# Performance work log

Measured on AMD Instinct MI355X. Metric: run time of the kernel, lower is better.

The kernel has to match this reference:

```python
import jax, jax.numpy as jnp
import numpy as np

B, L, A, HD, H = 4096, 512, 64, 1024, 32
EPS = 1e-5


def _ln(x, g, b):
    m = jnp.mean(x, axis=-1, keepdims=True)
    v = jnp.mean((x - m) ** 2, axis=-1, keepdims=True)
    return (x - m) * jax.lax.rsqrt(v + EPS) * g + b


def setup_inputs() -> dict:
    key = jax.random.key(0)
    ks = jax.random.split(key, 12)
    s = 0.02
    return {
        "z_0": jax.random.normal(ks[0], (B, L), jnp.float32),
        "actions": jax.random.normal(ks[1], (B, H, A), jnp.float32),
        "W1": jax.random.normal(ks[2], (L + A, HD), jnp.float32) * s,
        "b1": jnp.zeros((HD,), jnp.float32),
        "g1": jnp.ones((HD,), jnp.float32),
        "be1": jnp.zeros((HD,), jnp.float32),
        "W2": jax.random.normal(ks[3], (HD, HD), jnp.float32) * s,
        "b2": jnp.zeros((HD,), jnp.float32),
        "g2": jnp.ones((HD,), jnp.float32),
        "be2": jnp.zeros((HD,), jnp.float32),
        "W3": jax.random.normal(ks[4], (HD, L), jnp.float32) * s,
        "b3": jnp.zeros((L,), jnp.float32),
        "uW1": jax.random.normal(ks[5], (L, HD // 2), jnp.float32) * s,
        "ub1": jnp.zeros((HD // 2,), jnp.float32),
        "uW2": jax.random.normal(ks[6], (HD // 2, 1), jnp.float32) * s,
        "ub2": jnp.zeros((1,), jnp.float32),
        "gate": jnp.asarray(0.5, jnp.float32),
    }


def reference(z_0, actions, W1, b1, g1, be1, W2, b2, g2, be2, W3, b3,
              uW1, ub1, uW2, ub2, gate):
    gate_s = jax.nn.sigmoid(gate)

    def step_fn(z, a):
        za = jnp.concatenate([z, a], axis=-1)              # [B, L+A]
        h = jax.nn.gelu(_ln(za @ W1 + b1, g1, be1), approximate=False)
        h = jax.nn.gelu(_ln(h @ W2 + b2, g2, be2), approximate=False)
        dz = h @ W3 + b3                                   # [B, L]
        z_next = z + gate_s * dz
        u = jax.nn.gelu(z_next @ uW1 + ub1, approximate=False)
        sigma = jax.nn.softplus(u @ uW2 + ub2)             # [B, 1]
        return z_next, (z_next, sigma)

    a_seq = jnp.swapaxes(actions, 0, 1)                    # [H, B, A]
    _, (traj, sigs) = jax.lax.scan(step_fn, z_0, a_seq)
    return jnp.swapaxes(traj, 0, 1), jnp.swapaxes(sigs, 0, 1)
```

## Files before the change

kernel.cpp:

```cpp
#include <hip/hip_runtime.h>
#include <hip/hip_bf16.h>
#include <math.h>

#define B_SZ 4096
#define L_SZ 512
#define A_SZ 64
#define HD_SZ 1024
#define H_SZ 32

typedef __attribute__((ext_vector_type(8))) short bf16x8;
typedef __attribute__((ext_vector_type(4))) short s16x4;
typedef __attribute__((ext_vector_type(4))) float f32x4;

union frag_u { bf16x8 v; s16x4 h[2]; };

#define GLDS16(gsrc, ldst) __builtin_amdgcn_global_load_lds(              \
    (const __attribute__((address_space(1))) void*)(gsrc),                \
    (__attribute__((address_space(3))) void*)(ldst), 16, 0, 0)

__device__ __forceinline__ float gelu_exact(float x) {
  return 0.5f * x * (1.0f + erff(x * 0.70710678118654752f));
}

template <int BM, int BN, int MODE>
__global__ __launch_bounds__(256, 2) void gemm_kernel(
    const __hip_bfloat16* __restrict__ A0, int a0s,
    const __hip_bfloat16* __restrict__ A1, int a1s, int ksplit,
    const __hip_bfloat16* __restrict__ Bt,
    const float* __restrict__ bias,
    int N, int K,
    float* __restrict__ outf,
    float* __restrict__ z_cur,
    __hip_bfloat16* __restrict__ znb,
    float* __restrict__ traj,
    const float* __restrict__ gate,
    int t,
    const float* __restrict__ uW2,
    float* __restrict__ sig_acc) {
  constexpr int BK = 64;
  constexpr int FM = BM / 32, FN = BN / 32;
  constexpr int HALF = (BM + BN) * BK;
  __shared__ __align__(16) __hip_bfloat16 lds[2 * HALF];

  const int tid = threadIdx.x;
  const int m0 = blockIdx.x * BM, n0 = blockIdx.y * BN;
  const int wave = tid >> 6, lane = tid & 63;
  const int l15 = lane & 15, lg = lane >> 4;
  const int wm = wave >> 1, wn = wave & 1;
  const int NK = K / BK;

  f32x4 acc[FM][FN];
#pragma unroll
  for (int mi = 0; mi < FM; ++mi)
#pragma unroll
    for (int ni = 0; ni < FN; ++ni) acc[mi][ni] = (f32x4){0.f, 0.f, 0.f, 0.f};

  auto stage = [&](int buf, int kt) {
    __hip_bfloat16* dA = lds + buf * HALF;
    __hip_bfloat16* dB = dA + BM * BK;
    const int k0 = kt * BK;
    const __hip_bfloat16* Aptr;
    int As, kloc;
    if (k0 < ksplit) { Aptr = A0; As = a0s; kloc = k0; }
    else             { Aptr = A1; As = a1s; kloc = k0 - ksplit; }
#pragma unroll
    for (int i = 0; i < BM / 32; ++i) {
      int off = tid * 16 + i * 4096;
      int r = off >> 7, c = off & 127;
      int csw = c ^ ((r & 7) << 4);
      GLDS16(Aptr + (size_t)(m0 + r) * As + kloc + (csw >> 1), dA + (off >> 1));
    }
#pragma unroll
    for (int i = 0; i < BN / 32; ++i) {
      int off = tid * 16 + i * 4096;
      int r = off >> 7, c = off & 127;
      int csw = c ^ ((r & 7) << 4);
      GLDS16(Bt + (size_t)(n0 + r) * K + k0 + (csw >> 1), dB + (off >> 1));
    }
  };

  stage(0, 0);
  asm volatile("s_waitcnt vmcnt(0)" ::: "memory");
  __syncthreads();

  int buf = 0;
  for (int kt = 0; kt < NK; ++kt) {
    if (kt + 1 < NK) stage(buf ^ 1, kt + 1);

    const __hip_bfloat16* ldsA = lds + buf * HALF;
    const __hip_bfloat16* ldsB = ldsA + BM * BK;

    frag_u a_[FM][2], b_[FN][2];
#pragma unroll
    for (int mi = 0; mi < FM; ++mi) {
      int row = wm * (FM * 16) + mi * 16 + l15;
      int xr = (row & 7) << 4;
      const char* base = (const char*)(ldsA + row * BK);
#pragma unroll
      for (int s = 0; s < 2; ++s) {
        a_[mi][s].h[0] = *(const s16x4*)(base + ((s * 64 + lg * 8) ^ xr));
        a_[mi][s].h[1] = *(const s16x4*)(base + ((s * 64 + 32 + lg * 8) ^ xr));
      }
    }
#pragma unroll
    for (int ni = 0; ni < FN; ++ni) {
      int row = wn * (FN * 16) + ni * 16 + l15;
      int xr = (row & 7) << 4;
      const char* base = (const char*)(ldsB + row * BK);
#pragma unroll
      for (int s = 0; s < 2; ++s) {
        b_[ni][s].h[0] = *(const s16x4*)(base + ((s * 64 + lg * 8) ^ xr));
        b_[ni][s].h[1] = *(const s16x4*)(base + ((s * 64 + 32 + lg * 8) ^ xr));
      }
    }
#pragma unroll
    for (int s = 0; s < 2; ++s)
#pragma unroll
      for (int mi = 0; mi < FM; ++mi)
#pragma unroll
        for (int ni = 0; ni < FN; ++ni)
          acc[mi][ni] = __builtin_amdgcn_mfma_f32_16x16x32_bf16(
              a_[mi][s].v, b_[ni][s].v, acc[mi][ni], 0, 0, 0);

    asm volatile("s_waitcnt vmcnt(0)" ::: "memory");
    __syncthreads();
    buf ^= 1;
  }

  if constexpr (MODE == 3) {
#pragma unroll
    for (int mi = 0; mi < FM; ++mi) {
      float p[4] = {0.f, 0.f, 0.f, 0.f};
#pragma unroll
      for (int ni = 0; ni < FN; ++ni) {
        int gcol = n0 + wn * (FN * 16) + ni * 16 + l15;
        float bv = bias[gcol];
        float w2 = uW2[gcol];
#pragma unroll
        for (int r = 0; r < 4; ++r)
          p[r] += gelu_exact(acc[mi][ni][r] + bv) * w2;
      }
#pragma unroll
      for (int o = 1; o < 16; o <<= 1) {
#pragma unroll
        for (int r = 0; r < 4; ++r) p[r] += __shfl_xor(p[r], o);
      }
      if (l15 == 0) {
        int rowb = m0 + wm * (FM * 16) + mi * 16 + lg * 4;
#pragma unroll
        for (int r = 0; r < 4; ++r)
          atomicAdd(&sig_acc[(size_t)(rowb + r) * H_SZ + t], p[r]);
      }
    }
  } else {
    float gs = 0.f;
    if constexpr (MODE == 1) gs = 1.f / (1.f + expf(-gate[0]));
#pragma unroll
    for (int mi = 0; mi < FM; ++mi) {
#pragma unroll
      for (int ni = 0; ni < FN; ++ni) {
        int gcol = n0 + wn * (FN * 16) + ni * 16 + l15;
        float bv = bias[gcol];
#pragma unroll
        for (int r = 0; r < 4; ++r) {
          int grow = m0 + wm * (FM * 16) + mi * 16 + lg * 4 + r;
          float v = acc[mi][ni][r] + bv;
          if constexpr (MODE == 0) {
            outf[(size_t)grow * N + gcol] = v;
          } else {
            size_t zi = (size_t)grow * L_SZ + gcol;
            float zn = z_cur[zi] + gs * v;
            z_cur[zi] = zn;
            znb[zi] = __float2bfloat16(zn);
            traj[(size_t)grow * (H_SZ * L_SZ) + (size_t)t * L_SZ + gcol] = zn;
          }
        }
      }
    }
  }
}

__global__ __launch_bounds__(256) void ln_gelu_kernel(
    const float* __restrict__ x, const float* __restrict__ gam,
    const float* __restrict__ bet, __hip_bfloat16* __restrict__ out) {
  constexpr int N = HD_SZ;
  const int row = blockIdx.x;
  const int tid = threadIdx.x, lane = tid & 63, wave = tid >> 6;
  const float* xr = x + (size_t)row * N;
  f32x4 v = *(const f32x4*)(xr + tid * 4);
  float s = v[0] + v[1] + v[2] + v[3];
  float s2 = v[0] * v[0] + v[1] * v[1] + v[2] * v[2] + v[3] * v[3];
#pragma unroll
  for (int o = 32; o; o >>= 1) {
    s += __shfl_xor(s, o);
    s2 += __shfl_xor(s2, o);
  }
  __shared__ float as_[4], as2_[4];
  if (lane == 0) { as_[wave] = s; as2_[wave] = s2; }
  __syncthreads();
  s = as_[0] + as_[1] + as_[2] + as_[3];
  s2 = as2_[0] + as2_[1] + as2_[2] + as2_[3];
  float mean = s * (1.f / N);
  float var = s2 * (1.f / N) - mean * mean;
  float rstd = rsqrtf(var + 1e-5f);
  f32x4 g = *(const f32x4*)(gam + tid * 4);
  f32x4 b = *(const f32x4*)(bet + tid * 4);
  union { __hip_bfloat16 h[4]; s16x4 sv; } o;
#pragma unroll
  for (int j = 0; j < 4; ++j) {
    float y = (v[j] - mean) * rstd * g[j] + b[j];
    o.h[j] = __float2bfloat16(gelu_exact(y));
  }
  *(s16x4*)(out + (size_t)row * N + tid * 4) = o.sv;
}

__global__ void transpose_cvt(const float* __restrict__ in,
                              __hip_bfloat16* __restrict__ out, int K, int N) {
  __shared__ float tile[32][33];
  const int n0 = blockIdx.x * 32, k0 = blockIdx.y * 32;
  const int tx = threadIdx.x, ty = threadIdx.y;
#pragma unroll
  for (int i = 0; i < 32; i += 8)
    tile[ty + i][tx] = in[(size_t)(k0 + ty + i) * N + (n0 + tx)];
  __syncthreads();
#pragma unroll
  for (int i = 0; i < 32; i += 8)
    out[(size_t)(n0 + ty + i) * K + (k0 + tx)] = __float2bfloat16(tile[tx][ty + i]);
}

__global__ void cvt_bf16_kernel(const float* __restrict__ in,
                                __hip_bfloat16* __restrict__ out, int n4) {
  int i = blockIdx.x * 256 + threadIdx.x;
  if (i >= n4) return;
  f32x4 v = ((const f32x4*)in)[i];
  union { __hip_bfloat16 h[4]; s16x4 sv; } o;
#pragma unroll
  for (int j = 0; j < 4; ++j) o.h[j] = __float2bfloat16(v[j]);
  ((s16x4*)out)[i] = o.sv;
}

__global__ void init_z_kernel(const float* __restrict__ z0,
                              float* __restrict__ z_cur,
                              __hip_bfloat16* __restrict__ znb, int n4) {
  int i = blockIdx.x * 256 + threadIdx.x;
  if (i >= n4) return;
  f32x4 v = ((const f32x4*)z0)[i];
  ((f32x4*)z_cur)[i] = v;
  union { __hip_bfloat16 h[4]; s16x4 sv; } o;
#pragma unroll
  for (int j = 0; j < 4; ++j) o.h[j] = __float2bfloat16(v[j]);
  ((s16x4*)znb)[i] = o.sv;
}

__global__ void zero_kernel(float* __restrict__ p, int n) {
  int i = blockIdx.x * 256 + threadIdx.x;
  if (i < n) p[i] = 0.f;
}

__global__ void softplus_kernel(const float* __restrict__ acc,
                                const float* __restrict__ ub2,
                                float* __restrict__ out, int n) {
  int i = blockIdx.x * 256 + threadIdx.x;
  if (i >= n) return;
  float v = acc[i] + ub2[0];
  out[i] = v > 20.f ? v : log1pf(expf(v));
}

extern "C" void kernel_launch(void* const* d_in, const int* in_sizes, int n_in,
                              void* d_out, int out_size, void* d_ws,
                              size_t ws_size, hipStream_t stream) {
  const float* z0      = (const float*)d_in[0];
  const float* actions = (const float*)d_in[1];
  const float* W1  = (const float*)d_in[2];
  const float* b1  = (const float*)d_in[3];
  const float* g1  = (const float*)d_in[4];
  const float* be1 = (const float*)d_in[5];
  const float* W2  = (const float*)d_in[6];
  const float* b2  = (const float*)d_in[7];
  const float* g2  = (const float*)d_in[8];
  const float* be2 = (const float*)d_in[9];
  const float* W3  = (const float*)d_in[10];
  const float* b3  = (const float*)d_in[11];
  const float* uW1 = (const float*)d_in[12];
  const float* ub1 = (const float*)d_in[13];
  const float* uW2 = (const float*)d_in[14];
  const float* ub2 = (const float*)d_in[15];
  const float* gate = (const float*)d_in[16];

  char* w = (char*)d_ws;
  __hip_bfloat16* W1t = (__hip_bfloat16*)w;  w += (size_t)(L_SZ + A_SZ) * HD_SZ * 2;
  __hip_bfloat16* W2t = (__hip_bfloat16*)w;  w += (size_t)HD_SZ * HD_SZ * 2;
  __hip_bfloat16* W3t = (__hip_bfloat16*)w;  w += (size_t)HD_SZ * L_SZ * 2;
  __hip_bfloat16* uW1t = (__hip_bfloat16*)w; w += (size_t)L_SZ * (HD_SZ / 2) * 2;
  __hip_bfloat16* actb = (__hip_bfloat16*)w; w += (size_t)B_SZ * H_SZ * A_SZ * 2;
  float* z_cur = (float*)w;                  w += (size_t)B_SZ * L_SZ * 4;
  __hip_bfloat16* znb = (__hip_bfloat16*)w;  w += (size_t)B_SZ * L_SZ * 2;
  float* tws = (float*)w;                    w += (size_t)B_SZ * HD_SZ * 4;
  __hip_bfloat16* hb = (__hip_bfloat16*)w;   w += (size_t)B_SZ * HD_SZ * 2;
  float* sig_acc = (float*)w;                w += (size_t)B_SZ * H_SZ * 4;

  float* trajOut = (float*)d_out;
  float* sigsOut = (float*)d_out + (size_t)B_SZ * H_SZ * L_SZ;

  dim3 tb(32, 8);
  transpose_cvt<<<dim3(HD_SZ / 32, (L_SZ + A_SZ) / 32), tb, 0, stream>>>(W1, W1t, L_SZ + A_SZ, HD_SZ);
  transpose_cvt<<<dim3(HD_SZ / 32, HD_SZ / 32), tb, 0, stream>>>(W2, W2t, HD_SZ, HD_SZ);
  transpose_cvt<<<dim3(L_SZ / 32, HD_SZ / 32), tb, 0, stream>>>(W3, W3t, HD_SZ, L_SZ);
  transpose_cvt<<<dim3((HD_SZ / 2) / 32, L_SZ / 32), tb, 0, stream>>>(uW1, uW1t, L_SZ, HD_SZ / 2);

  cvt_bf16_kernel<<<(B_SZ * H_SZ * A_SZ / 4 + 255) / 256, 256, 0, stream>>>(
      actions, actb, B_SZ * H_SZ * A_SZ / 4);
  init_z_kernel<<<(B_SZ * L_SZ / 4 + 255) / 256, 256, 0, stream>>>(
      z0, z_cur, znb, B_SZ * L_SZ / 4);
  zero_kernel<<<(B_SZ * H_SZ + 255) / 256, 256, 0, stream>>>(sig_acc, B_SZ * H_SZ);

  const int KSPLIT_NONE = 1 << 30;
  for (int t = 0; t < H_SZ; ++t) {
    gemm_kernel<64, 128, 0><<<dim3(B_SZ / 64, HD_SZ / 128), 256, 0, stream>>>(
        znb, L_SZ, actb + (size_t)t * A_SZ, H_SZ * A_SZ, L_SZ, W1t, b1,
        HD_SZ, L_SZ + A_SZ, tws, nullptr, nullptr, nullptr, nullptr, 0,
        nullptr, nullptr);
    ln_gelu_kernel<<<B_SZ, 256, 0, stream>>>(tws, g1, be1, hb);
    gemm_kernel<64, 128, 0><<<dim3(B_SZ / 64, HD_SZ / 128), 256, 0, stream>>>(
        hb, HD_SZ, nullptr, 0, KSPLIT_NONE, W2t, b2,
        HD_SZ, HD_SZ, tws, nullptr, nullptr, nullptr, nullptr, 0,
        nullptr, nullptr);
    ln_gelu_kernel<<<B_SZ, 256, 0, stream>>>(tws, g2, be2, hb);
    gemm_kernel<32, 128, 1><<<dim3(B_SZ / 32, L_SZ / 128), 256, 0, stream>>>(
        hb, HD_SZ, nullptr, 0, KSPLIT_NONE, W3t, b3,
        L_SZ, HD_SZ, nullptr, z_cur, znb, trajOut, gate, t,
        nullptr, nullptr);
    gemm_kernel<32, 128, 3><<<dim3(B_SZ / 32, (HD_SZ / 2) / 128), 256, 0, stream>>>(
        znb, L_SZ, nullptr, 0, KSPLIT_NONE, uW1t, ub1,
        HD_SZ / 2, L_SZ, nullptr, nullptr, nullptr, nullptr, nullptr, t,
        uW2, sig_acc);
  }
  softplus_kernel<<<(B_SZ * H_SZ + 255) / 256, 256, 0, stream>>>(
      sig_acc, ub2, sigsOut, B_SZ * H_SZ);
}
```

Baseline: 2.518 ms.

## Switch GEMM to triple-buffered BK=32 pipeline with counted waits and larger tiles

Restructures the GEMM main loop from a double-buffered BK=64 scheme to a three-stage LDS ring with BK=32. It issues loads two tiles ahead and uses counted vmcnt waits instead of draining all outstanding loads each iteration. LDS fragment reads become single 16-byte loads with a simpler swizzle, and all four GEMM launches double their M tile (128x128 and 64x128). The aim is to keep more global loads in flight and raise MFMA work per block, at the cost of more barriers per K step and fewer blocks in each grid.

```diff
diff --git a/kernel.cpp b/kernel.cpp
--- a/kernel.cpp
+++ b/kernel.cpp
@@ -12,11 +12,13 @@
 typedef __attribute__((ext_vector_type(4))) short s16x4;
 typedef __attribute__((ext_vector_type(4))) float f32x4;
 
-union frag_u { bf16x8 v; s16x4 h[2]; };
-
 #define GLDS16(gsrc, ldst) __builtin_amdgcn_global_load_lds(              \
     (const __attribute__((address_space(1))) void*)(gsrc),                \
     (__attribute__((address_space(3))) void*)(ldst), 16, 0, 0)
+
+template <int N> __device__ __forceinline__ void vmwait() {
+  asm volatile("s_waitcnt vmcnt(%0)" :: "n"(N) : "memory");
+}
 
 __device__ __forceinline__ float gelu_exact(float x) {
   return 0.5f * x * (1.0f + erff(x * 0.70710678118654752f));
@@ -37,10 +39,12 @@
     int t,
     const float* __restrict__ uW2,
     float* __restrict__ sig_acc) {
-  constexpr int BK = 64;
+  constexpr int BK = 32;
   constexpr int FM = BM / 32, FN = BN / 32;
-  constexpr int HALF = (BM + BN) * BK;
-  __shared__ __align__(16) __hip_bfloat16 lds[2 * HALF];
+  constexpr int ABYTES = BM * 64;
+  constexpr int BUFB = (BM + BN) * 64;
+  constexpr int LOADS = (BM + BN) / 64;
+  __shared__ __align__(16) char lds[3 * BUFB];
 
   const int tid = threadIdx.x;
   const int m0 = blockIdx.x * BM, n0 = blockIdx.y * BN;
@@ -56,75 +60,65 @@
     for (int ni = 0; ni < FN; ++ni) acc[mi][ni] = (f32x4){0.f, 0.f, 0.f, 0.f};
 
   auto stage = [&](int buf, int kt) {
-    __hip_bfloat16* dA = lds + buf * HALF;
-    __hip_bfloat16* dB = dA + BM * BK;
+    char* dst = lds + buf * BUFB;
     const int k0 = kt * BK;
     const __hip_bfloat16* Aptr;
     int As, kloc;
     if (k0 < ksplit) { Aptr = A0; As = a0s; kloc = k0; }
     else             { Aptr = A1; As = a1s; kloc = k0 - ksplit; }
 #pragma unroll
-    for (int i = 0; i < BM / 32; ++i) {
+    for (int i = 0; i < BM / 64; ++i) {
       int off = tid * 16 + i * 4096;
-      int r = off >> 7, c = off & 127;
-      int csw = c ^ ((r & 7) << 4);
-      GLDS16(Aptr + (size_t)(m0 + r) * As + kloc + (csw >> 1), dA + (off >> 1));
-    }
-#pragma unroll
-    for (int i = 0; i < BN / 32; ++i) {
+      int r = off >> 6;
+      int csw = (off & 63) ^ ((r & 3) << 4);
+      GLDS16(Aptr + (size_t)(m0 + r) * As + kloc + (csw >> 1), dst + off);
+    }
+#pragma unroll
+    for (int i = 0; i < BN / 64; ++i) {
       int off = tid * 16 + i * 4096;
-      int r = off >> 7, c = off & 127;
-      int csw = c ^ ((r & 7) << 4);
-      GLDS16(Bt + (size_t)(n0 + r) * K + k0 + (csw >> 1), dB + (off >> 1));
+      int r = off >> 6;
+      int csw = (off & 63) ^ ((r & 3) << 4);
+      GLDS16(Bt + (size_t)(n0 + r) * K + k0 + (csw >> 1), dst + ABYTES + off);
     }
   };
 
+  const int xr = (l15 & 3) << 4;
+  const int abase = (wm * (FM * 16) + l15) * 64 + ((lg * 16) ^ xr);
+  const int bbase = ABYTES + (wn * (FN * 16) + l15) * 64 + ((lg * 16) ^ xr);
+
   stage(0, 0);
-  asm volatile("s_waitcnt vmcnt(0)" ::: "memory");
-  __syncthreads();
+  stage(1, 1);
 
   int buf = 0;
   for (int kt = 0; kt < NK; ++kt) {
-    if (kt + 1 < NK) stage(buf ^ 1, kt + 1);
-
-    const __hip_bfloat16* ldsA = lds + buf * HALF;
-    const __hip_bfloat16* ldsB = ldsA + BM * BK;
-
-    frag_u a_[FM][2], b_[FN][2];
-#pragma unroll
-    for (int mi = 0; mi < FM; ++mi) {
-      int row = wm * (FM * 16) + mi * 16 + l15;
-      int xr = (row & 7) << 4;
-      const char* base = (const char*)(ldsA + row * BK);
-#pragma unroll
-      for (int s = 0; s < 2; ++s) {
-        a_[mi][s].h[0] = *(const s16x4*)(base + ((s * 64 + lg * 8) ^ xr));
-        a_[mi][s].h[1] = *(const s16x4*)(base + ((s * 64 + 32 + lg * 8) ^ xr));
-      }
-    }
-#pragma unroll
-    for (int ni = 0; ni < FN; ++ni) {
-      int row = wn * (FN * 16) + ni * 16 + l15;
-      int xr = (row & 7) << 4;
-      const char* base = (const char*)(ldsB + row * BK);
-#pragma unroll
-      for (int s = 0; s < 2; ++s) {
-        b_[ni][s].h[0] = *(const s16x4*)(base + ((s * 64 + lg * 8) ^ xr));
-        b_[ni][s].h[1] = *(const s16x4*)(base + ((s * 64 + 32 + lg * 8) ^ xr));
-      }
-    }
-#pragma unroll
-    for (int s = 0; s < 2; ++s)
-#pragma unroll
-      for (int mi = 0; mi < FM; ++mi)
-#pragma unroll
-        for (int ni = 0; ni < FN; ++ni)
-          acc[mi][ni] = __builtin_amdgcn_mfma_f32_16x16x32_bf16(
-              a_[mi][s].v, b_[ni][s].v, acc[mi][ni], 0, 0, 0);
-
-    asm volatile("s_waitcnt vmcnt(0)" ::: "memory");
-    __syncthreads();
-    buf ^= 1;
+    if (kt + 2 < NK) {
+      int b2 = buf + 2; if (b2 >= 3) b2 -= 3;
+      stage(b2, kt + 2);
+    }
+    if (kt + 2 < NK)      vmwait<2 * LOADS>();
+    else if (kt + 1 < NK) vmwait<LOADS>();
+    else                  vmwait<0>();
+    __builtin_amdgcn_s_barrier();
+    asm volatile("" ::: "memory");
+
+    const char* lb = lds + buf * BUFB;
+    bf16x8 a_[FM], b_[FN];
+#pragma unroll
+    for (int mi = 0; mi < FM; ++mi)
+      a_[mi] = *(const bf16x8*)(lb + abase + mi * 1024);
+#pragma unroll
+    for (int ni = 0; ni < FN; ++ni)
+      b_[ni] = *(const bf16x8*)(lb + bbase + ni * 1024);
+#pragma unroll
+    for (int mi = 0; mi < FM; ++mi)
+#pragma unroll
+      for (int ni = 0; ni < FN; ++ni)
+        acc[mi][ni] = __builtin_amdgcn_mfma_f32_16x16x32_bf16(
+            a_[mi], b_[ni], acc[mi][ni], 0, 0, 0);
+
+    asm volatile("" ::: "memory");
+    __builtin_amdgcn_s_barrier();
+    buf = (buf + 1 == 3) ? 0 : buf + 1;
   }
 
   if constexpr (MODE == 3) {
@@ -316,21 +310,21 @@
 
   const int KSPLIT_NONE = 1 << 30;
   for (int t = 0; t < H_SZ; ++t) {
-    gemm_kernel<64, 128, 0><<<dim3(B_SZ / 64, HD_SZ / 128), 256, 0, stream>>>(
+    gemm_kernel<128, 128, 0><<<dim3(B_SZ / 128, HD_SZ / 128), 256, 0, stream>>>(
         znb, L_SZ, actb + (size_t)t * A_SZ, H_SZ * A_SZ, L_SZ, W1t, b1,
         HD_SZ, L_SZ + A_SZ, tws, nullptr, nullptr, nullptr, nullptr, 0,
         nullptr, nullptr);
     ln_gelu_kernel<<<B_SZ, 256, 0, stream>>>(tws, g1, be1, hb);
-    gemm_kernel<64, 128, 0><<<dim3(B_SZ / 64, HD_SZ / 128), 256, 0, stream>>>(
+    gemm_kernel<128, 128, 0><<<dim3(B_SZ / 128, HD_SZ / 128), 256, 0, stream>>>(
         hb, HD_SZ, nullptr, 0, KSPLIT_NONE, W2t, b2,
         HD_SZ, HD_SZ, tws, nullptr, nullptr, nullptr, nullptr, 0,
         nullptr, nullptr);
     ln_gelu_kernel<<<B_SZ, 256, 0, stream>>>(tws, g2, be2, hb);
-    gemm_kernel<32, 128, 1><<<dim3(B_SZ / 32, L_SZ / 128), 256, 0, stream>>>(
+    gemm_kernel<64, 128, 1><<<dim3(B_SZ / 64, L_SZ / 128), 256, 0, stream>>>(
         hb, HD_SZ, nullptr, 0, KSPLIT_NONE, W3t, b3,
         L_SZ, HD_SZ, nullptr, z_cur, znb, trajOut, gate, t,
         nullptr, nullptr);
-    gemm_kernel<32, 128, 3><<<dim3(B_SZ / 32, (HD_SZ / 2) / 128), 256, 0, stream>>>(
+    gemm_kernel<64, 128, 3><<<dim3(B_SZ / 64, (HD_SZ / 2) / 128), 256, 0, stream>>>(
         znb, L_SZ, nullptr, 0, KSPLIT_NONE, uW1t, ub1,
         HD_SZ / 2, L_SZ, nullptr, nullptr, nullptr, nullptr, nullptr, t,
         uW2, sig_acc);
```

After: 2.642 ms. 1.05x slower.

## Fold uncertainty-head projection into W3 GEMM via precomposed W3·uW1 weights

Applied to the files above, without the earlier changes.

The product W3·uW1 and the matching bias term are precomputed once, so each step runs a single N=1024 GEMM. It produces both dz and the increment of z·uW1, and a running fp32 pre-activation buffer zu is kept. This removes the separate per-step uW1 GEMM, its launch and its re-read of the bf16 state. The cost is more GEMM work per step, an extra fp32 read-modify-write of zu, and drift between zu and the bf16 state. The LDS fragment loads also change from two 8-byte reads to one 16-byte read per MFMA operand.

```diff
diff --git a/kernel.cpp b/kernel.cpp
--- a/kernel.cpp
+++ b/kernel.cpp
@@ -11,8 +11,6 @@
 typedef __attribute__((ext_vector_type(8))) short bf16x8;
 typedef __attribute__((ext_vector_type(4))) short s16x4;
 typedef __attribute__((ext_vector_type(4))) float f32x4;
-
-union frag_u { bf16x8 v; s16x4 h[2]; };
 
 #define GLDS16(gsrc, ldst) __builtin_amdgcn_global_load_lds(              \
     (const __attribute__((address_space(1))) void*)(gsrc),                \
@@ -35,12 +33,16 @@
     float* __restrict__ traj,
     const float* __restrict__ gate,
     int t,
+    float* __restrict__ zu,
+    const float* __restrict__ ub1v,
     const float* __restrict__ uW2,
     float* __restrict__ sig_acc) {
   constexpr int BK = 64;
+  constexpr int ROWB = BK * 2;
   constexpr int FM = BM / 32, FN = BN / 32;
-  constexpr int HALF = (BM + BN) * BK;
-  __shared__ __align__(16) __hip_bfloat16 lds[2 * HALF];
+  constexpr int ABYTES = BM * ROWB;
+  constexpr int BUFB = (BM + BN) * ROWB;
+  __shared__ __align__(16) char lds[2 * BUFB];
 
   const int tid = threadIdx.x;
   const int m0 = blockIdx.x * BM, n0 = blockIdx.y * BN;
@@ -56,8 +58,7 @@
     for (int ni = 0; ni < FN; ++ni) acc[mi][ni] = (f32x4){0.f, 0.f, 0.f, 0.f};
 
   auto stage = [&](int buf, int kt) {
-    __hip_bfloat16* dA = lds + buf * HALF;
-    __hip_bfloat16* dB = dA + BM * BK;
+    char* dst = lds + buf * BUFB;
     const int k0 = kt * BK;
     const __hip_bfloat16* Aptr;
     int As, kloc;
@@ -66,18 +67,23 @@
 #pragma unroll
     for (int i = 0; i < BM / 32; ++i) {
       int off = tid * 16 + i * 4096;
-      int r = off >> 7, c = off & 127;
-      int csw = c ^ ((r & 7) << 4);
-      GLDS16(Aptr + (size_t)(m0 + r) * As + kloc + (csw >> 1), dA + (off >> 1));
+      int r = off >> 7;
+      int csw = (off & 127) ^ ((r & 7) << 4);
+      GLDS16(Aptr + (size_t)(m0 + r) * As + kloc + (csw >> 1), dst + off);
     }
 #pragma unroll
     for (int i = 0; i < BN / 32; ++i) {
       int off = tid * 16 + i * 4096;
-      int r = off >> 7, c = off & 127;
-      int csw = c ^ ((r & 7) << 4);
-      GLDS16(Bt + (size_t)(n0 + r) * K + k0 + (csw >> 1), dB + (off >> 1));
+      int r = off >> 7;
+      int csw = (off & 127) ^ ((r & 7) << 4);
+      GLDS16(Bt + (size_t)(n0 + r) * K + k0 + (csw >> 1), dst + ABYTES + off);
     }
   };
+
+  const int xrow = (l15 & 7) << 4;
+  const int offs0 = (lg * 16) ^ xrow;
+  const int aoff = (wm * (FM * 16) + l15) * ROWB;
+  const int boff = ABYTES + (wn * (FN * 16) + l15) * ROWB;
 
   stage(0, 0);
   asm volatile("s_waitcnt vmcnt(0)" ::: "memory");
@@ -87,31 +93,17 @@
   for (int kt = 0; kt < NK; ++kt) {
     if (kt + 1 < NK) stage(buf ^ 1, kt + 1);
 
-    const __hip_bfloat16* ldsA = lds + buf * HALF;
-    const __hip_bfloat16* ldsB = ldsA + BM * BK;
-
-    frag_u a_[FM][2], b_[FN][2];
+    const char* lb = lds + buf * BUFB;
+    bf16x8 a_[FM][2], b_[FN][2];
 #pragma unroll
     for (int mi = 0; mi < FM; ++mi) {
-      int row = wm * (FM * 16) + mi * 16 + l15;
-      int xr = (row & 7) << 4;
-      const char* base = (const char*)(ldsA + row * BK);
-#pragma unroll
-      for (int s = 0; s < 2; ++s) {
-        a_[mi][s].h[0] = *(const s16x4*)(base + ((s * 64 + lg * 8) ^ xr));
-        a_[mi][s].h[1] = *(const s16x4*)(base + ((s * 64 + 32 + lg * 8) ^ xr));
-      }
+      a_[mi][0] = *(const bf16x8*)(lb + aoff + mi * (16 * ROWB) + offs0);
+      a_[mi][1] = *(const bf16x8*)(lb + aoff + mi * (16 * ROWB) + (offs0 ^ 64));
     }
 #pragma unroll
     for (int ni = 0; ni < FN; ++ni) {
-      int row = wn * (FN * 16) + ni * 16 + l15;
-      int xr = (row & 7) << 4;
-      const char* base = (const char*)(ldsB + row * BK);
-#pragma unroll
-      for (int s = 0; s < 2; ++s) {
-        b_[ni][s].h[0] = *(const s16x4*)(base + ((s * 64 + lg * 8) ^ xr));
-        b_[ni][s].h[1] = *(const s16x4*)(base + ((s * 64 + 32 + lg * 8) ^ xr));
-      }
+      b_[ni][0] = *(const bf16x8*)(lb + boff + ni * (16 * ROWB) + offs0);
+      b_[ni][1] = *(const bf16x8*)(lb + boff + ni * (16 * ROWB) + (offs0 ^ 64));
     }
 #pragma unroll
     for (int s = 0; s < 2; ++s)
@@ -120,60 +112,77 @@
 #pragma unroll
         for (int ni = 0; ni < FN; ++ni)
           acc[mi][ni] = __builtin_amdgcn_mfma_f32_16x16x32_bf16(
-              a_[mi][s].v, b_[ni][s].v, acc[mi][ni], 0, 0, 0);
+              a_[mi][s], b_[ni][s], acc[mi][ni], 0, 0, 0);
 
     asm volatile("s_waitcnt vmcnt(0)" ::: "memory");
     __syncthreads();
     buf ^= 1;
   }
 
-  if constexpr (MODE == 3) {
+  if constexpr (MODE == 0) {
 #pragma unroll
     for (int mi = 0; mi < FM; ++mi) {
-      float p[4] = {0.f, 0.f, 0.f, 0.f};
 #pragma unroll
       for (int ni = 0; ni < FN; ++ni) {
         int gcol = n0 + wn * (FN * 16) + ni * 16 + l15;
         float bv = bias[gcol];
-        float w2 = uW2[gcol];
-#pragma unroll
-        for (int r = 0; r < 4; ++r)
-          p[r] += gelu_exact(acc[mi][ni][r] + bv) * w2;
-      }
-#pragma unroll
-      for (int o = 1; o < 16; o <<= 1) {
-#pragma unroll
-        for (int r = 0; r < 4; ++r) p[r] += __shfl_xor(p[r], o);
-      }
-      if (l15 == 0) {
-        int rowb = m0 + wm * (FM * 16) + mi * 16 + lg * 4;
-#pragma unroll
-        for (int r = 0; r < 4; ++r)
-          atomicAdd(&sig_acc[(size_t)(rowb + r) * H_SZ + t], p[r]);
-      }
-    }
-  } else {
-    float gs = 0.f;
-    if constexpr (MODE == 1) gs = 1.f / (1.f + expf(-gate[0]));
-#pragma unroll
-    for (int mi = 0; mi < FM; ++mi) {
-#pragma unroll
-      for (int ni = 0; ni < FN; ++ni) {
-        int gcol = n0 + wn * (FN * 16) + ni * 16 + l15;
-        float bv = bias[gcol];
 #pragma unroll
         for (int r = 0; r < 4; ++r) {
           int grow = m0 + wm * (FM * 16) + mi * 16 + lg * 4 + r;
-          float v = acc[mi][ni][r] + bv;
-          if constexpr (MODE == 0) {
-            outf[(size_t)grow * N + gcol] = v;
-          } else {
+          outf[(size_t)grow * N + gcol] = acc[mi][ni][r] + bv;
+        }
+      }
+    }
+  } else {
+    const float gs = 1.f / (1.f + expf(-gate[0]));
+    if (n0 < L_SZ) {
+#pragma unroll
+      for (int mi = 0; mi < FM; ++mi) {
+#pragma unroll
+        for (int ni = 0; ni < FN; ++ni) {
+          int gcol = n0 + wn * (FN * 16) + ni * 16 + l15;
+          float bv = bias[gcol];
+#pragma unroll
+          for (int r = 0; r < 4; ++r) {
+            int grow = m0 + wm * (FM * 16) + mi * 16 + lg * 4 + r;
             size_t zi = (size_t)grow * L_SZ + gcol;
-            float zn = z_cur[zi] + gs * v;
+            float zn = z_cur[zi] + gs * (acc[mi][ni][r] + bv);
             z_cur[zi] = zn;
             znb[zi] = __float2bfloat16(zn);
             traj[(size_t)grow * (H_SZ * L_SZ) + (size_t)t * L_SZ + gcol] = zn;
           }
+        }
+      }
+    } else {
+#pragma unroll
+      for (int mi = 0; mi < FM; ++mi) {
+        float p[4] = {0.f, 0.f, 0.f, 0.f};
+#pragma unroll
+        for (int ni = 0; ni < FN; ++ni) {
+          int gcol = n0 + wn * (FN * 16) + ni * 16 + l15;
+          int j = gcol - L_SZ;
+          float bv = bias[gcol];
+          float ub = ub1v[j];
+          float w2 = uW2[j];
+#pragma unroll
+          for (int r = 0; r < 4; ++r) {
+            int grow = m0 + wm * (FM * 16) + mi * 16 + lg * 4 + r;
+            size_t ui = (size_t)grow * L_SZ + j;
+            float zun = zu[ui] + gs * (acc[mi][ni][r] + bv);
+            zu[ui] = zun;
+            p[r] += gelu_exact(zun + ub) * w2;
+          }
+        }
+#pragma unroll
+        for (int o = 1; o < 16; o <<= 1) {
+#pragma unroll
+          for (int r = 0; r < 4; ++r) p[r] += __shfl_xor(p[r], o);
+        }
+        if (l15 == 0) {
+          int rowb = m0 + wm * (FM * 16) + mi * 16 + lg * 4;
+#pragma unroll
+          for (int r = 0; r < 4; ++r)
+            atomicAdd(&sig_acc[(size_t)(rowb + r) * H_SZ + t], p[r]);
         }
       }
     }
@@ -226,6 +235,36 @@
 #pragma unroll
   for (int i = 0; i < 32; i += 8)
     out[(size_t)(n0 + ty + i) * K + (k0 + tx)] = __float2bfloat16(tile[tx][ty + i]);
+}
+
+__global__ __launch_bounds__(256) void w34_kernel(
+    const float* __restrict__ W3, const float* __restrict__ uW1,
+    __hip_bfloat16* __restrict__ W3c) {
+  __shared__ float tA[16][17];
+  __shared__ float tB[16][17];
+  const int k0 = blockIdx.x * 16, j0 = blockIdx.y * 16;
+  const int tx = threadIdx.x & 15, ty = threadIdx.x >> 4;
+  float acc = 0.f;
+  for (int i0 = 0; i0 < L_SZ; i0 += 16) {
+    tA[ty][tx] = W3[(size_t)(k0 + ty) * L_SZ + i0 + tx];
+    tB[ty][tx] = uW1[(size_t)(i0 + ty) * (HD_SZ / 2) + j0 + tx];
+    __syncthreads();
+#pragma unroll
+    for (int i = 0; i < 16; ++i) acc += tA[ty][i] * tB[i][tx];
+    __syncthreads();
+  }
+  W3c[(size_t)(L_SZ + j0 + tx) * HD_SZ + k0 + ty] = __float2bfloat16(acc);
+}
+
+__global__ void bias3_kernel(const float* __restrict__ b3,
+                             const float* __restrict__ uW1,
+                             float* __restrict__ bias3c) {
+  int j = blockIdx.x * 256 + threadIdx.x;
+  if (j >= L_SZ) return;
+  bias3c[j] = b3[j];
+  float s = 0.f;
+  for (int i = 0; i < L_SZ; ++i) s += b3[i] * uW1[(size_t)i * (HD_SZ / 2) + j];
+  bias3c[L_SZ + j] = s;
 }
 
 __global__ void cvt_bf16_kernel(const float* __restrict__ in,
@@ -290,14 +329,17 @@
   char* w = (char*)d_ws;
   __hip_bfloat16* W1t = (__hip_bfloat16*)w;  w += (size_t)(L_SZ + A_SZ) * HD_SZ * 2;
   __hip_bfloat16* W2t = (__hip_bfloat16*)w;  w += (size_t)HD_SZ * HD_SZ * 2;
-  __hip_bfloat16* W3t = (__hip_bfloat16*)w;  w += (size_t)HD_SZ * L_SZ * 2;
+  __hip_bfloat16* W3c = (__hip_bfloat16*)w;  w += (size_t)HD_SZ * HD_SZ * 2;
   __hip_bfloat16* uW1t = (__hip_bfloat16*)w; w += (size_t)L_SZ * (HD_SZ / 2) * 2;
   __hip_bfloat16* actb = (__hip_bfloat16*)w; w += (size_t)B_SZ * H_SZ * A_SZ * 2;
   float* z_cur = (float*)w;                  w += (size_t)B_SZ * L_SZ * 4;
   __hip_bfloat16* znb = (__hip_bfloat16*)w;  w += (size_t)B_SZ * L_SZ * 2;
+  float* zu = (float*)w;                     w += (size_t)B_SZ * L_SZ * 4;
   float* tws = (float*)w;                    w += (size_t)B_SZ * HD_SZ * 4;
   __hip_bfloat16* hb = (__hip_bfloat16*)w;   w += (size_t)B_SZ * HD_SZ * 2;
   float* sig_acc = (float*)w;                w += (size_t)B_SZ * H_SZ * 4;
+  float* bias3c = (float*)w;                 w += (size_t)HD_SZ * 4;
+  float* zbias = (float*)w;                  w += (size_t)L_SZ * 4;
 
   float* trajOut = (float*)d_out;
   float* sigsOut = (float*)d_out + (size_t)B_SZ * H_SZ * L_SZ;
@@ -305,35 +347,41 @@
   dim3 tb(32, 8);
   transpose_cvt<<<dim3(HD_SZ / 32, (L_SZ + A_SZ) / 32), tb, 0, stream>>>(W1, W1t, L_SZ + A_SZ, HD_SZ);
   transpose_cvt<<<dim3(HD_SZ / 32, HD_SZ / 32), tb, 0, stream>>>(W2, W2t, HD_SZ, HD_SZ);
-  transpose_cvt<<<dim3(L_SZ / 32, HD_SZ / 32), tb, 0, stream>>>(W3, W3t, HD_SZ, L_SZ);
+  transpose_cvt<<<dim3(L_SZ / 32, HD_SZ / 32), tb, 0, stream>>>(W3, W3c, HD_SZ, L_SZ);
   transpose_cvt<<<dim3((HD_SZ / 2) / 32, L_SZ / 32), tb, 0, stream>>>(uW1, uW1t, L_SZ, HD_SZ / 2);
+  w34_kernel<<<dim3(HD_SZ / 16, L_SZ / 16), 256, 0, stream>>>(W3, uW1, W3c);
+  bias3_kernel<<<2, 256, 0, stream>>>(b3, uW1, bias3c);
 
   cvt_bf16_kernel<<<(B_SZ * H_SZ * A_SZ / 4 + 255) / 256, 256, 0, stream>>>(
       actions, actb, B_SZ * H_SZ * A_SZ / 4);
   init_z_kernel<<<(B_SZ * L_SZ / 4 + 255) / 256, 256, 0, stream>>>(
       z0, z_cur, znb, B_SZ * L_SZ / 4);
-  zero_kernel<<<(B_SZ * H_SZ + 255) / 256, 256, 0, stream>>>(sig_acc, B_SZ * H_SZ);
+  zero_kernel<<<(B_SZ * H_SZ + L_SZ + 255) / 256, 256, 0, stream>>>(
+      sig_acc, B_SZ * H_SZ + L_SZ);
+  zero_kernel<<<(L_SZ + 255) / 256, 256, 0, stream>>>(zbias, L_SZ);
 
   const int KSPLIT_NONE = 1 << 30;
+
+  gemm_kernel<64, 128, 0><<<dim3(B_SZ / 64, L_SZ / 128), 256, 0, stream>>>(
+      znb, L_SZ, nullptr, 0, KSPLIT_NONE, uW1t, zbias,
+      L_SZ, L_SZ, zu, nullptr, nullptr, nullptr, nullptr, 0,
+      nullptr, nullptr, nullptr, nullptr);
+
   for (int t = 0; t < H_SZ; ++t) {
     gemm_kernel<64, 128, 0><<<dim3(B_SZ / 64, HD_SZ / 128), 256, 0, stream>>>(
         znb, L_SZ, actb + (size_t)t * A_SZ, H_SZ * A_SZ, L_SZ, W1t, b1,
         HD_SZ, L_SZ + A_SZ, tws, nullptr, nullptr, nullptr, nullptr, 0,
-        nullptr, nullptr);
+        nullptr, nullptr, nullptr, nullptr);
     ln_gelu_kernel<<<B_SZ, 256, 0, stream>>>(tws, g1, be1, hb);
     gemm_kernel<64, 128, 0><<<dim3(B_SZ / 64, HD_SZ / 128), 256, 0, stream>>>(
         hb, HD_SZ, nullptr, 0, KSPLIT_NONE, W2t, b2,
         HD_SZ, HD_SZ, tws, nullptr, nullptr, nullptr, nullptr, 0,
-        nullptr, nullptr);
+        nullptr, nullptr, nullptr, nullptr);
     ln_gelu_kernel<<<B_SZ, 256, 0, stream>>>(tws, g2, be2, hb);
-    gemm_kernel<32, 128, 1><<<dim3(B_SZ / 32, L_SZ / 128), 256, 0, stream>>>(
-        hb, HD_SZ, nullptr, 0, KSPLIT_NONE, W3t, b3,
-        L_SZ, HD_SZ, nullptr, z_cur, znb, trajOut, gate, t,
-        nullptr, nullptr);
-    gemm_kernel<32, 128, 3><<<dim3(B_SZ / 32, (HD_SZ / 2) / 128), 256, 0, stream>>>(
-        znb, L_SZ, nullptr, 0, KSPLIT_NONE, uW1t, ub1,
-        HD_SZ / 2, L_SZ, nullptr, nullptr, nullptr, nullptr, nullptr, t,
-        uW2, sig_acc);
+    gemm_kernel<64, 128, 4><<<dim3(B_SZ / 64, HD_SZ / 128), 256, 0, stream>>>(
+        hb, HD_SZ, nullptr, 0, KSPLIT_NONE, W3c, bias3c,
+        HD_SZ, HD_SZ, nullptr, z_cur, znb, trajOut, gate, t,
+        zu, ub1, uW2, sig_acc);
   }
   softplus_kernel<<<(B_SZ * H_SZ + 255) / 256, 256, 0, stream>>>(
       sig_acc, ub2, sigsOut, B_SZ * H_SZ);
```

After: 2.384 ms. 5.3% less time.
